# Optimization experiments

Hardware: AMD Instinct MI355X
Metric: run time of the kernel (lower is better)

The kernel has to match this reference:

```python
import jax, jax.numpy as jnp
import numpy as np

NHEAD = 16
EPS = 1e-5

def layer_norm(x, g, b):
    mu = jnp.mean(x, axis=-1, keepdims=True)
    var = jnp.mean(jnp.square(x - mu), axis=-1, keepdims=True)
    return (x - mu) * jax.lax.rsqrt(var + EPS) * g + b

def setup_inputs() -> dict:
    key = jax.random.key(0)
    ks = jax.random.split(key, 12)
    d_model, d_hid = 1024, 4096  # MHA num_hiddens == dim_feedforward (source quirk)
    B, S = 2, 2048
    s_in = 1.0 / np.sqrt(d_model)
    s_hid = 1.0 / np.sqrt(d_hid)
    return {
        "x": jax.random.normal(ks[0], (B, S, d_model), jnp.float32),
        "Wq": jax.random.normal(ks[1], (d_model, d_hid), jnp.float32) * s_in,
        "Wk": jax.random.normal(ks[2], (d_model, d_hid), jnp.float32) * s_in,
        "Wv": jax.random.normal(ks[3], (d_model, d_hid), jnp.float32) * s_in,
        "Wo": jax.random.normal(ks[4], (d_hid, d_model), jnp.float32) * s_hid,
        "W1": jax.random.normal(ks[5], (d_model, d_hid), jnp.float32) * s_in,
        "b1": jnp.zeros((d_hid,), jnp.float32),
        "W2": jax.random.normal(ks[6], (d_hid, d_model), jnp.float32) * s_hid,
        "b2": jnp.zeros((d_model,), jnp.float32),
        "g1": jnp.ones((d_model,), jnp.float32),
        "be1": jnp.zeros((d_model,), jnp.float32),
        "g2": jnp.ones((d_model,), jnp.float32),
        "be2": jnp.zeros((d_model,), jnp.float32),
    }

def reference(x, Wq, Wk, Wv, Wo, W1, b1, W2, b2, g1, be1, g2, be2):
    B, S, D = x.shape
    H = NHEAD
    # pre-norm attention branch (dropout = identity at eval)
    x1 = layer_norm(x, g1, be1)
    q = (x1 @ Wq).reshape(B, S, H, -1)  # [B,S,H,dh], dh = num_hiddens/H
    k = (x1 @ Wk).reshape(B, S, H, -1)
    v = (x1 @ Wv).reshape(B, S, H, -1)
    dh = q.shape[-1]
    scores = jnp.einsum('bqhd,bkhd->bhqk', q, k) / jnp.sqrt(jnp.float32(dh))
    attn = jax.nn.softmax(scores, axis=-1)
    ctx = jnp.einsum('bhqk,bkhd->bqhd', attn, v).reshape(B, S, -1)
    x = x + ctx @ Wo
    # pre-norm FFN branch
    x2 = layer_norm(x, g2, be2)
    h = jax.nn.relu(x2 @ W1 + b1)
    out = x + (h @ W2 + b2)
    return out
```

## Files before the change

### kernel.cpp

```cpp
#include <hip/hip_runtime.h>
#include <hip/hip_bf16.h>
#include <stdint.h>

using bf16x8 = __attribute__((ext_vector_type(8))) __bf16;
using f32x4  = __attribute__((ext_vector_type(4))) float;

__device__ __forceinline__ uint16_t f2bf(float f) {
    uint32_t u = __builtin_bit_cast(uint32_t, f);
    u += 0x7FFFu + ((u >> 16) & 1u);
    return (uint16_t)(u >> 16);
}
__device__ __forceinline__ uint32_t pack2bf(float lo, float hi) {
    return (uint32_t)f2bf(lo) | ((uint32_t)f2bf(hi) << 16);
}

__device__ __forceinline__ void gld_lds16(const void* g, void* l) {
    __builtin_amdgcn_global_load_lds(
        (const __attribute__((address_space(1))) void*)g,
        (__attribute__((address_space(3))) void*)l,
        16, 0, 0);
}

__global__ __launch_bounds__(256)
void wconvB(const float* __restrict__ i0, const float* __restrict__ i1,
            const float* __restrict__ i2, uint16_t* __restrict__ o0,
            uint16_t* __restrict__ o1, uint16_t* __restrict__ o2,
            int R, int C) {
    int z = blockIdx.z;
    const float* in = z == 0 ? i0 : (z == 1 ? i1 : i2);
    uint16_t* out   = z == 0 ? o0 : (z == 1 ? o1 : o2);
    __shared__ float t[32][33];
    int c0 = blockIdx.x * 32, r0 = blockIdx.y * 32;
    int tx = threadIdx.x & 31, ty = threadIdx.x >> 5;
    #pragma unroll
    for (int i = 0; i < 32; i += 8)
        t[ty + i][tx] = in[(size_t)(r0 + ty + i) * C + c0 + tx];
    __syncthreads();
    #pragma unroll
    for (int i = 0; i < 32; i += 8)
        out[(size_t)(c0 + ty + i) * R + r0 + tx] = f2bf(t[tx][ty + i]);
}

__global__ __launch_bounds__(256)
void ln_bf16(const float* __restrict__ x, const float* __restrict__ gw,
             const float* __restrict__ bw, uint16_t* __restrict__ out) {
    const int D = 1024;
    int row = blockIdx.x;
    float4 v = ((const float4*)(x + (size_t)row * D))[threadIdx.x];
    float s  = v.x + v.y + v.z + v.w;
    float ss = v.x * v.x + v.y * v.y + v.z * v.z + v.w * v.w;
    #pragma unroll
    for (int m = 1; m < 64; m <<= 1) {
        s  += __shfl_xor(s, m);
        ss += __shfl_xor(ss, m);
    }
    __shared__ float red[8];
    int wid = threadIdx.x >> 6, lane = threadIdx.x & 63;
    if (lane == 0) { red[wid] = s; red[4 + wid] = ss; }
    __syncthreads();
    s  = red[0] + red[1] + red[2] + red[3];
    ss = red[4] + red[5] + red[6] + red[7];
    float mu  = s * (1.f / 1024.f);
    float var = ss * (1.f / 1024.f) - mu * mu;
    float rstd = rsqrtf(var + 1e-5f);
    float4 gv = ((const float4*)gw)[threadIdx.x];
    float4 bv = ((const float4*)bw)[threadIdx.x];
    ushort4 o;
    o.x = f2bf((v.x - mu) * rstd * gv.x + bv.x);
    o.y = f2bf((v.y - mu) * rstd * gv.y + bv.y);
    o.z = f2bf((v.z - mu) * rstd * gv.z + bv.z);
    o.w = f2bf((v.w - mu) * rstd * gv.w + bv.w);
    ((ushort4*)(out + (size_t)row * D))[threadIdx.x] = o;
}

template <int EPI>
__global__ __launch_bounds__(256, 2)
void gemm128p(const uint16_t* __restrict__ A, const uint16_t* __restrict__ B,
              void* __restrict__ Cp, const float* __restrict__ bias,
              const float* __restrict__ resid, int M, int N, int K) {
    __shared__ uint8_t smem[65536];
    int bid = blockIdx.x;
    int cpx = gridDim.x >> 3;
    bid = (bid & 7) * cpx + (bid >> 3);
    int nbn  = N >> 7;
    int brow = (bid / nbn) << 7;
    int bcol = (bid % nbn) << 7;
    int t0 = threadIdx.x;
    int wid = t0 >> 6, lane = t0 & 63;
    int wr = wid >> 1, wc = wid & 1;
    int q = lane & 15, g = lane >> 4;

    const uint16_t* Asw = A + (size_t)(brow + (lane >> 3)) * K + (((lane & 7) ^ (lane >> 3)) << 3);
    const uint16_t* Bsw = B + (size_t)(bcol + (lane >> 3)) * K + (((lane & 7) ^ (lane >> 3)) << 3);

    f32x4 acc[4][4] = {};
    int NKT = K >> 6;

#define STG128(BSEL, KK)                                                       \
    {                                                                          \
        uint8_t* dA = smem + (BSEL) * 16384;                                   \
        uint8_t* dB = smem + 32768 + (BSEL) * 16384;                           \
        _Pragma("unroll")                                                      \
        for (int i = 0; i < 4; ++i) {                                          \
            int c = wid * 4 + i;                                               \
            gld_lds16(Asw + (size_t)(c * 8) * K + (KK), dA + c * 1024);        \
            gld_lds16(Bsw + (size_t)(c * 8) * K + (KK), dB + c * 1024);        \
        }                                                                      \
    }

    STG128(0, 0)

    for (int t = 0; t < NKT; ++t) {
        int cur = t & 1;
        if (t + 1 < NKT) {
            STG128(cur ^ 1, (t + 1) << 6)
            asm volatile("s_waitcnt vmcnt(8)" ::: "memory");
        } else {
            asm volatile("s_waitcnt vmcnt(0)" ::: "memory");
        }
        __builtin_amdgcn_sched_barrier(0);
        __builtin_amdgcn_s_barrier();
        __builtin_amdgcn_sched_barrier(0);

        const uint8_t* bA = smem + cur * 16384;
        const uint8_t* bB = smem + 32768 + cur * 16384;

        bf16x8 af[4][2], bfr[4][2];
        #pragma unroll
        for (int m2 = 0; m2 < 4; ++m2)
            #pragma unroll
            for (int ks = 0; ks < 2; ++ks) {
                int rr = wr * 64 + m2 * 16 + q;
                int sl = (ks * 4 + g) ^ (q & 7);
                af[m2][ks] = *(const bf16x8*)(bA + rr * 128 + sl * 16);
            }
        #pragma unroll
        for (int n2 = 0; n2 < 4; ++n2)
            #pragma unroll
            for (int ks = 0; ks < 2; ++ks) {
                int cc = wc * 64 + n2 * 16 + q;
                int sl = (ks * 4 + g) ^ (q & 7);
                bfr[n2][ks] = *(const bf16x8*)(bB + cc * 128 + sl * 16);
            }
        __builtin_amdgcn_s_setprio(1);
        #pragma unroll
        for (int m2 = 0; m2 < 4; ++m2)
            #pragma unroll
            for (int n2 = 0; n2 < 4; ++n2)
                #pragma unroll
                for (int ks = 0; ks < 2; ++ks)
                    acc[m2][n2] = __builtin_amdgcn_mfma_f32_16x16x32_bf16(
                        af[m2][ks], bfr[n2][ks], acc[m2][n2], 0, 0, 0);
        __builtin_amdgcn_s_setprio(0);
        __builtin_amdgcn_s_barrier();
    }

    uint16_t* Cb = (uint16_t*)Cp;
    float*    Cf = (float*)Cp;
    #pragma unroll
    for (int m2 = 0; m2 < 4; ++m2)
        #pragma unroll
        for (int n2 = 0; n2 < 4; ++n2)
            #pragma unroll
            for (int r = 0; r < 4; ++r) {
                int gr = brow + wr * 64 + m2 * 16 + g * 4 + r;
                int gc = bcol + wc * 64 + n2 * 16 + q;
                float v = acc[m2][n2][r];
                size_t idx = (size_t)gr * N + gc;
                if constexpr (EPI == 0) {
                    Cb[idx] = f2bf(v);
                } else if constexpr (EPI == 1) {
                    v += bias[gc];
                    Cb[idx] = f2bf(v > 0.f ? v : 0.f);
                } else if constexpr (EPI == 2) {
                    Cf[idx] = v + bias[gc] + resid[idx];
                } else {
                    Cf[idx] = v + resid[idx];
                }
            }
#undef STG128
}

__device__ __forceinline__ void attn_stage(uint8_t* smem, int bufsel,
        const uint16_t* Kb0, const uint16_t* Vb0, int ktok, int wid, int lane) {
    #pragma unroll
    for (int i = 0; i < 4; ++i) {
        int chunk = wid * 4 + i;
        int r = 2 * chunk + (lane >> 5);
        int s = lane & 31;
        int cg = (s & ~7) | ((s ^ r) & 7);
        gld_lds16(Kb0 + (size_t)(ktok + r) * 8192 + cg * 8,
                  smem + bufsel * 16384 + chunk * 1024);
    }
    #pragma unroll
    for (int i = 0; i < 4; ++i) {
        int chunk = wid * 4 + i;
        int r = 16 * chunk + (lane >> 2);
        int s = lane & 3;
        int cg = s ^ (r & 3);
        gld_lds16(Vb0 + (size_t)r * 4096 + ktok + cg * 8,
                  smem + 32768 + bufsel * 16384 + chunk * 1024);
    }
}

__device__ __forceinline__ bf16x8 sm_pack(const f32x4* sacc, f32x4* acc,
                                          float& m_run, float& l_run,
                                          int q, int g) {
    float mx = fmaxf(fmaxf(fmaxf(sacc[0][0], sacc[0][1]), fmaxf(sacc[0][2], sacc[0][3])),
                     fmaxf(fmaxf(sacc[1][0], sacc[1][1]), fmaxf(sacc[1][2], sacc[1][3])));
    mx = fmaxf(mx, __shfl_xor(mx, 16));
    mx = fmaxf(mx, __shfl_xor(mx, 32));
    if (!__all(mx - m_run <= 8.f)) {
        float m_new = fmaxf(m_run, mx);
        float alpha = __expf(m_run - m_new);
        l_run *= alpha;
        #pragma unroll
        for (int td = 0; td < 16; ++td) {
            acc[td][0] *= alpha; acc[td][1] *= alpha;
            acc[td][2] *= alpha; acc[td][3] *= alpha;
        }
        m_run = m_new;
    }
    float p[8]; float rs = 0.f;
    #pragma unroll
    for (int tm = 0; tm < 2; ++tm)
        #pragma unroll
        for (int r = 0; r < 4; ++r) {
            float e = __expf(sacc[tm][r] - m_run);
            p[tm * 4 + r] = e; rs += e;
        }
    l_run += rs;

    uint32_t pk0 = pack2bf(p[0], p[1]);
    uint32_t pk1 = pack2bf(p[2], p[3]);
    uint32_t pk2 = pack2bf(p[4], p[5]);
    uint32_t pk3 = pack2bf(p[6], p[7]);
    int srcA = ((g & 1) << 5) + q;
    int srcB = srcA + 16;
    uint32_t a0 = __shfl(pk0, srcA), a1 = __shfl(pk2, srcA);
    uint32_t b0 = __shfl(pk1, srcA), b1 = __shfl(pk3, srcA);
    uint32_t c0 = __shfl(pk0, srcB), c1 = __shfl(pk2, srcB);
    uint32_t d0 = __shfl(pk1, srcB), d1 = __shfl(pk3, srcB);
    bool hi = g >= 2;
    uint4 pb;
    pb.x = hi ? a1 : a0;
    pb.y = hi ? b1 : b0;
    pb.z = hi ? c1 : c0;
    pb.w = hi ? d1 : d0;
    return __builtin_bit_cast(bf16x8, pb);
}

__global__ __launch_bounds__(256, 2)
void attn(const uint16_t* __restrict__ Qg, const uint16_t* __restrict__ Kg,
          const uint16_t* __restrict__ Vtg, uint16_t* __restrict__ Og) {
    const int S = 2048, NT = 64, QKS = 8192, OC = 4096;
    __shared__ uint8_t smem[65536];

    int id = blockIdx.x;
    id = (id & 7) * 64 + (id >> 3);
    int qb = id & 15, h = (id >> 4) & 15, b = id >> 8;

    int t = threadIdx.x;
    int wid = t >> 6, lane = t & 63;
    int q = lane & 15, g = lane >> 4;
    int tok0 = b * S + qb * 128 + wid * 32;

    bf16x8 qf0[8], qf1[8];
    {
        const uint16_t* qrow0 = Qg + (size_t)(tok0 + q) * QKS + h * 256 + g * 8;
        const uint16_t* qrow1 = Qg + (size_t)(tok0 + 16 + q) * QKS + h * 256 + g * 8;
        #pragma unroll
        for (int c = 0; c < 8; ++c) {
            bf16x8 r0 = *(const bf16x8*)(qrow0 + c * 32);
            bf16x8 r1 = *(const bf16x8*)(qrow1 + c * 32);
            #pragma unroll
            for (int i = 0; i < 8; ++i) {
                r0[i] = (__bf16)((float)r0[i] * 0.0625f);
                r1[i] = (__bf16)((float)r1[i] * 0.0625f);
            }
            qf0[c] = r0; qf1[c] = r1;
        }
    }

    f32x4 acc0[16] = {}, acc1[16] = {};
    float m0 = -1e30f, l0 = 0.f;
    float m1 = -1e30f, l1 = 0.f;

    const uint16_t* Kb0 = Kg + (size_t)(b * S) * QKS + h * 256;
    const uint16_t* Vb0 = Vtg + (size_t)(h * 256) * 4096 + b * S;

    attn_stage(smem, 0, Kb0, Vb0, 0, wid, lane);

    for (int kt = 0; kt < NT; ++kt) {
        int cb = (kt & 1) * 16384;
        if (kt + 1 < NT) {
            attn_stage(smem, (kt + 1) & 1, Kb0, Vb0, (kt + 1) * 32, wid, lane);
            asm volatile("s_waitcnt vmcnt(8)" ::: "memory");
        } else {
            asm volatile("s_waitcnt vmcnt(0)" ::: "memory");
        }
        __builtin_amdgcn_sched_barrier(0);
        __builtin_amdgcn_s_barrier();

        const uint16_t* sk = (const uint16_t*)(smem + cb);
        const uint16_t* sv = (const uint16_t*)(smem + 32768 + cb);

        f32x4 sA0[2] = {}, sA1[2] = {};
        __builtin_amdgcn_s_setprio(1);
        #pragma unroll
        for (int c = 0; c < 8; ++c) {
            #pragma unroll
            for (int tm = 0; tm < 2; ++tm) {
                int G = c * 4 + g;
                int slot = (G & ~7) | ((G ^ q) & 7);
                bf16x8 kf = *(const bf16x8*)(sk + (tm * 16 + q) * 256 + slot * 8);
                sA0[tm] = __builtin_amdgcn_mfma_f32_16x16x32_bf16(kf, qf0[c], sA0[tm], 0, 0, 0);
                sA1[tm] = __builtin_amdgcn_mfma_f32_16x16x32_bf16(kf, qf1[c], sA1[tm], 0, 0, 0);
            }
        }
        __builtin_amdgcn_s_setprio(0);

        bf16x8 pfrag0 = sm_pack(sA0, acc0, m0, l0, q, g);
        bf16x8 pfrag1 = sm_pack(sA1, acc1, m1, l1, q, g);

        int sl = g ^ (q & 3);
        __builtin_amdgcn_s_setprio(1);
        #pragma unroll
        for (int td = 0; td < 16; ++td) {
            bf16x8 vf = *(const bf16x8*)(sv + (td * 16 + q) * 32 + sl * 8);
            acc0[td] = __builtin_amdgcn_mfma_f32_16x16x32_bf16(vf, pfrag0, acc0[td], 0, 0, 0);
            acc1[td] = __builtin_amdgcn_mfma_f32_16x16x32_bf16(vf, pfrag1, acc1[td], 0, 0, 0);
        }
        __builtin_amdgcn_s_setprio(0);
        __builtin_amdgcn_s_barrier();
    }

    l0 += __shfl_xor(l0, 16); l0 += __shfl_xor(l0, 32);
    l1 += __shfl_xor(l1, 16); l1 += __shfl_xor(l1, 32);

    __syncthreads();
    {
        float inv0 = 1.f / l0, inv1 = 1.f / l1;
        uint32_t* w0 = (uint32_t*)(smem + wid * 16384);
        uint32_t* w1 = (uint32_t*)(smem + wid * 16384 + 8192);
        #pragma unroll
        for (int td = 0; td < 16; ++td) {
            int base = (q * 256 + td * 16 + g * 4) >> 1;
            w0[base]     = pack2bf(acc0[td][0] * inv0, acc0[td][1] * inv0);
            w0[base + 1] = pack2bf(acc0[td][2] * inv0, acc0[td][3] * inv0);
            w1[base]     = pack2bf(acc1[td][0] * inv1, acc1[td][1] * inv1);
            w1[base + 1] = pack2bf(acc1[td][2] * inv1, acc1[td][3] * inv1);
        }
    }
    __syncthreads();
    #pragma unroll
    for (int s2 = 0; s2 < 2; ++s2) {
        const uint16_t* tb = (const uint16_t*)(smem + wid * 16384 + s2 * 8192);
        #pragma unroll
        for (int r2 = 0; r2 < 8; ++r2) {
            int c = r2 * 64 + lane;
            int qq = c >> 5, dc = c & 31;
            uint4 v = *(const uint4*)&tb[qq * 256 + dc * 8];
            *(uint4*)(Og + (size_t)(tok0 + s2 * 16 + qq) * OC + h * 256 + dc * 8) = v;
        }
    }
}

extern "C" void kernel_launch(void* const* d_in, const int* in_sizes, int n_in,
                              void* d_out, int out_size, void* d_ws, size_t ws_size,
                              hipStream_t stream) {
    const float* x   = (const float*)d_in[0];
    const float* Wq  = (const float*)d_in[1];
    const float* Wk  = (const float*)d_in[2];
    const float* Wv  = (const float*)d_in[3];
    const float* Wo  = (const float*)d_in[4];
    const float* W1  = (const float*)d_in[5];
    const float* b1  = (const float*)d_in[6];
    const float* W2  = (const float*)d_in[7];
    const float* b2  = (const float*)d_in[8];
    const float* g1  = (const float*)d_in[9];
    const float* be1 = (const float*)d_in[10];
    const float* g2  = (const float*)d_in[11];
    const float* be2 = (const float*)d_in[12];

    char* ws = (char*)d_ws;
    const size_t M8 = 8388608;
    uint16_t* WqkT = (uint16_t*)(ws + 0 * M8);
    uint16_t* WqT  = WqkT;
    uint16_t* WkT  = (uint16_t*)(ws + 1 * M8);
    uint16_t* WvT  = (uint16_t*)(ws + 2 * M8);
    uint16_t* WoT  = (uint16_t*)(ws + 3 * M8);
    uint16_t* W1T  = (uint16_t*)(ws + 4 * M8);
    uint16_t* W2T  = (uint16_t*)(ws + 5 * M8);
    uint16_t* x1   = (uint16_t*)(ws + 6 * M8);
    uint16_t* x2   = (uint16_t*)(ws + 7 * M8);
    uint16_t* QK   = (uint16_t*)(ws + 8 * M8);
    uint16_t* Vt   = (uint16_t*)(ws + 16 * M8);
    uint16_t* ctx  = (uint16_t*)(ws + 20 * M8);
    float*    xmid = (float*)(ws + 12 * M8);
    uint16_t* Hn   = (uint16_t*)(ws + 8 * M8);

    wconvB<<<dim3(128, 32, 3), 256, 0, stream>>>(Wq, Wk, Wv, WqT, WkT, WvT, 1024, 4096);
    wconvB<<<dim3(32, 128, 2), 256, 0, stream>>>(Wo, W2, nullptr, WoT, W2T, nullptr, 4096, 1024);
    wconvB<<<dim3(128, 32, 1), 256, 0, stream>>>(W1, nullptr, nullptr, W1T, nullptr, nullptr, 1024, 4096);

    ln_bf16<<<4096, 256, 0, stream>>>(x, g1, be1, x1);

    gemm128p<0><<<2048, 256, 0, stream>>>(x1, WqkT, QK, nullptr, nullptr, 4096, 8192, 1024);
    gemm128p<0><<<1024, 256, 0, stream>>>(WvT, x1, Vt, nullptr, nullptr, 4096, 4096, 1024);

    attn<<<512, 256, 0, stream>>>(QK, QK + 4096, Vt, ctx);

    gemm128p<3><<<256, 256, 0, stream>>>(ctx, WoT, xmid, nullptr, x, 4096, 1024, 4096);

    ln_bf16<<<4096, 256, 0, stream>>>(xmid, g2, be2, x2);

    gemm128p<1><<<1024, 256, 0, stream>>>(x2, W1T, Hn, b1, nullptr, 4096, 4096, 1024);
    gemm128p<2><<<256, 256, 0, stream>>>(Hn, W2T, d_out, b2, xmid, 4096, 1024, 4096);
}
```

Baseline: 508.3 us.

## Add 256x128-tile GEMM with K=32 stages for bf16-output projections

Introduces a new gemmBig kernel that computes 256x128 output tiles per block (8x4 MFMA tiles per wave) with a 32-wide K step and double-buffered LDS, and uses it for the Q/K, V and W1 GEMMs. The larger M tile halves the number of blocks and increases arithmetic intensity per LDS load of B. The shorter K step doubles the number of barrier iterations, and the bigger accumulator array raises register pressure, which may limit occupancy at two blocks per CU. gemm128p is kept only for the fp32-output residual GEMMs.

```diff
diff --git a/kernel.cpp b/kernel.cpp
--- a/kernel.cpp
+++ b/kernel.cpp
@@ -76,7 +76,7 @@
 template <int EPI>
 __global__ __launch_bounds__(256, 2)
 void gemm128p(const uint16_t* __restrict__ A, const uint16_t* __restrict__ B,
-              void* __restrict__ Cp, const float* __restrict__ bias,
+              float* __restrict__ Cf, const float* __restrict__ bias,
               const float* __restrict__ resid, int M, int N, int K) {
     __shared__ uint8_t smem[65536];
     int bid = blockIdx.x;
@@ -155,8 +155,6 @@
         __builtin_amdgcn_s_barrier();
     }
 
-    uint16_t* Cb = (uint16_t*)Cp;
-    float*    Cf = (float*)Cp;
     #pragma unroll
     for (int m2 = 0; m2 < 4; ++m2)
         #pragma unroll
@@ -167,18 +165,112 @@
                 int gc = bcol + wc * 64 + n2 * 16 + q;
                 float v = acc[m2][n2][r];
                 size_t idx = (size_t)gr * N + gc;
-                if constexpr (EPI == 0) {
-                    Cb[idx] = f2bf(v);
-                } else if constexpr (EPI == 1) {
-                    v += bias[gc];
-                    Cb[idx] = f2bf(v > 0.f ? v : 0.f);
-                } else if constexpr (EPI == 2) {
+                if constexpr (EPI == 2) {
                     Cf[idx] = v + bias[gc] + resid[idx];
                 } else {
                     Cf[idx] = v + resid[idx];
                 }
             }
 #undef STG128
+}
+
+template <int EPI>
+__global__ __launch_bounds__(256, 2)
+void gemmBig(const uint16_t* __restrict__ A, const uint16_t* __restrict__ B,
+             void* __restrict__ Cp, const float* __restrict__ bias,
+             int M, int N, int K) {
+    __shared__ uint8_t smem[49152];
+    int bid = blockIdx.x;
+    int cpx = gridDim.x >> 3;
+    bid = (bid & 7) * cpx + (bid >> 3);
+    int nbn  = N >> 7;
+    int brow = (bid / nbn) << 8;
+    int bcol = (bid % nbn) << 7;
+    int t0 = threadIdx.x;
+    int wid = t0 >> 6, lane = t0 & 63;
+    int wr = wid >> 1, wc = wid & 1;
+    int q = lane & 15, g = lane >> 4;
+
+    int kswz = ((lane & 3) ^ ((lane >> 3) & 3)) << 3;
+    const uint16_t* Asw = A + (size_t)(brow + (lane >> 2)) * K + kswz;
+    const uint16_t* Bsw = B + (size_t)(bcol + (lane >> 2)) * K + kswz;
+
+    f32x4 acc[8][4] = {};
+    int NKT = K >> 5;
+
+#define STGBIG(BSEL, KK)                                                       \
+    {                                                                          \
+        uint8_t* dA = smem + (BSEL) * 16384;                                   \
+        uint8_t* dB = smem + 32768 + (BSEL) * 8192;                            \
+        _Pragma("unroll")                                                      \
+        for (int i = 0; i < 4; ++i) {                                          \
+            int c = wid * 4 + i;                                               \
+            gld_lds16(Asw + (size_t)(c * 16) * K + (KK), dA + c * 1024);       \
+        }                                                                      \
+        _Pragma("unroll")                                                      \
+        for (int i = 0; i < 2; ++i) {                                          \
+            int c = wid * 2 + i;                                               \
+            gld_lds16(Bsw + (size_t)(c * 16) * K + (KK), dB + c * 1024);       \
+        }                                                                      \
+    }
+
+    STGBIG(0, 0)
+
+    for (int t = 0; t < NKT; ++t) {
+        int cur = t & 1;
+        if (t + 1 < NKT) {
+            STGBIG(cur ^ 1, (t + 1) << 5)
+            asm volatile("s_waitcnt vmcnt(6)" ::: "memory");
+        } else {
+            asm volatile("s_waitcnt vmcnt(0)" ::: "memory");
+        }
+        __builtin_amdgcn_sched_barrier(0);
+        __builtin_amdgcn_s_barrier();
+        __builtin_amdgcn_sched_barrier(0);
+
+        const uint8_t* bA = smem + cur * 16384;
+        const uint8_t* bB = smem + 32768 + cur * 8192;
+        int sl = (g ^ ((q >> 1) & 3)) << 4;
+
+        bf16x8 af[8], bfr[4];
+        #pragma unroll
+        for (int m8 = 0; m8 < 8; ++m8) {
+            int rr = wr * 128 + m8 * 16 + q;
+            af[m8] = *(const bf16x8*)(bA + rr * 64 + sl);
+        }
+        #pragma unroll
+        for (int n4 = 0; n4 < 4; ++n4) {
+            int cc = wc * 64 + n4 * 16 + q;
+            bfr[n4] = *(const bf16x8*)(bB + cc * 64 + sl);
+        }
+        __builtin_amdgcn_s_setprio(1);
+        #pragma unroll
+        for (int m8 = 0; m8 < 8; ++m8)
+            #pragma unroll
+            for (int n4 = 0; n4 < 4; ++n4)
+                acc[m8][n4] = __builtin_amdgcn_mfma_f32_16x16x32_bf16(
+                    af[m8], bfr[n4], acc[m8][n4], 0, 0, 0);
+        __builtin_amdgcn_s_setprio(0);
+        __builtin_amdgcn_s_barrier();
+    }
+
+    uint16_t* Cb = (uint16_t*)Cp;
+    #pragma unroll
+    for (int m8 = 0; m8 < 8; ++m8)
+        #pragma unroll
+        for (int n4 = 0; n4 < 4; ++n4)
+            #pragma unroll
+            for (int r = 0; r < 4; ++r) {
+                int gr = brow + wr * 128 + m8 * 16 + g * 4 + r;
+                int gc = bcol + wc * 64 + n4 * 16 + q;
+                float v = acc[m8][n4][r];
+                if constexpr (EPI == 1) {
+                    v += bias[gc];
+                    v = v > 0.f ? v : 0.f;
+                }
+                Cb[(size_t)gr * N + gc] = f2bf(v);
+            }
+#undef STGBIG
 }
 
 __device__ __forceinline__ void attn_stage(uint8_t* smem, int bufsel,
@@ -406,8 +498,8 @@
 
     ln_bf16<<<4096, 256, 0, stream>>>(x, g1, be1, x1);
 
-    gemm128p<0><<<2048, 256, 0, stream>>>(x1, WqkT, QK, nullptr, nullptr, 4096, 8192, 1024);
-    gemm128p<0><<<1024, 256, 0, stream>>>(WvT, x1, Vt, nullptr, nullptr, 4096, 4096, 1024);
+    gemmBig<0><<<1024, 256, 0, stream>>>(x1, WqkT, QK, nullptr, 4096, 8192, 1024);
+    gemmBig<0><<<512, 256, 0, stream>>>(WvT, x1, Vt, nullptr, 4096, 4096, 1024);
 
     attn<<<512, 256, 0, stream>>>(QK, QK + 4096, Vt, ctx);
 
@@ -415,6 +507,6 @@
 
     ln_bf16<<<4096, 256, 0, stream>>>(xmid, g2, be2, x2);
 
-    gemm128p<1><<<1024, 256, 0, stream>>>(x2, W1T, Hn, b1, nullptr, 4096, 4096, 1024);
-    gemm128p<2><<<256, 256, 0, stream>>>(Hn, W2T, d_out, b2, xmid, 4096, 1024, 4096);
-}
+    gemmBig<1><<<512, 256, 0, stream>>>(x2, W1T, Hn, b1, 4096, 4096, 1024);
+    gemm128p<2><<<256, 256, 0, stream>>>(Hn, W2T, (float*)d_out, b2, xmid, 4096, 1024, 4096);
+}
```

Measured after the change: 471.5 us. 7.2% less time.
